# Optimization experiments

Hardware: AMD Instinct MI355X
Metric: run time of the kernel (lower is better)

The kernel has to match this reference:

```python
import jax, jax.numpy as jnp
import numpy as np
import math

WH, WW = 7, 7          # window size
N = WH * WW            # tokens per window = 49
H = 12                 # num heads
C = 384                # dim
D = C // H             # head dim = 32
NW = 64                # num windows (56x56 map, 7x7 windows)
B = 32                 # image batch
BW = B * NW            # windowed batch = 2048


def _cpb_constants():
    # log-spaced continuous relative coords table, flattened to [(2*WH-1)*(2*WW-1), 2]
    rh = np.arange(-(WH - 1), WH, dtype=np.float32)
    rw = np.arange(-(WW - 1), WW, dtype=np.float32)
    t = np.stack(np.meshgrid(rh, rw, indexing='ij'), axis=-1)  # [13,13,2]
    t[..., 0] /= (WH - 1)
    t[..., 1] /= (WW - 1)
    t *= 8.0
    t = np.sign(t) * np.log2(np.abs(t) + 1.0) / np.log2(8.0)
    # relative position index [N*N]
    ch, cw = np.meshgrid(np.arange(WH), np.arange(WW), indexing='ij')
    cf = np.stack([ch.ravel(), cw.ravel()])            # [2, N]
    rel = cf[:, :, None] - cf[:, None, :]              # [2, N, N]
    rel = rel.transpose(1, 2, 0).astype(np.int64)      # [N, N, 2]
    rel[..., 0] += WH - 1
    rel[..., 1] += WW - 1
    rel[..., 0] *= 2 * WW - 1
    rpi = rel.sum(-1).reshape(-1)                      # [N*N]
    return jnp.asarray(t.reshape(-1, 2)), jnp.asarray(rpi)

_COORDS_TABLE, _RPI = _cpb_constants()


def setup_inputs() -> dict:
    key = jax.random.key(0)
    ks = jax.random.split(key, 8)
    x = jax.random.normal(ks[0], (BW, N, C), dtype=jnp.float32)
    # shifted-window style 0/-100 mask
    mask = jnp.where(jax.random.uniform(ks[1], (NW, N, N)) < 0.1, -100.0, 0.0).astype(jnp.float32)
    qkv_w = jax.random.normal(ks[2], (3 * C, C), dtype=jnp.float32) * 0.02
    q_bias = jnp.zeros((C,), dtype=jnp.float32)
    v_bias = jnp.zeros((C,), dtype=jnp.float32)
    logit_scale = jnp.full((H, 1, 1), math.log(10.0), dtype=jnp.float32)
    cpb_w1 = jax.random.normal(ks[3], (512, 2), dtype=jnp.float32) * 0.02
    cpb_b1 = jnp.zeros((512,), dtype=jnp.float32)
    cpb_w2 = jax.random.normal(ks[4], (H, 512), dtype=jnp.float32) * 0.02
    proj_w = jax.random.normal(ks[5], (C, C), dtype=jnp.float32) * 0.02
    proj_b = jnp.zeros((C,), dtype=jnp.float32)
    return {"x": x, "mask": mask, "qkv_w": qkv_w, "q_bias": q_bias, "v_bias": v_bias,
            "logit_scale": logit_scale, "cpb_w1": cpb_w1, "cpb_b1": cpb_b1,
            "cpb_w2": cpb_w2, "proj_w": proj_w, "proj_b": proj_b}


def reference(x, mask, qkv_w, q_bias, v_bias, logit_scale, cpb_w1, cpb_b1, cpb_w2, proj_w, proj_b):
    B_, n, c = x.shape
    # qkv projection; k has no bias (registered zeros buffer)
    qkv_bias = jnp.concatenate([q_bias, jnp.zeros_like(q_bias), v_bias])
    qkv = x @ qkv_w.T + qkv_bias                              # [B_, N, 3C]
    qkv = qkv.reshape(B_, n, 3, H, D).transpose(2, 0, 3, 1, 4)  # [3, B_, H, N, D]
    q, k, v = qkv[0], qkv[1], qkv[2]
    # cosine attention
    qn = q / jnp.clip(jnp.linalg.norm(q, axis=-1, keepdims=True), 1e-12)
    kn = k / jnp.clip(jnp.linalg.norm(k, axis=-1, keepdims=True), 1e-12)
    attn = jnp.einsum('bhnd,bhmd->bhnm', qn, kn)              # [B_, H, N, N]
    scale = jnp.exp(jnp.minimum(logit_scale, math.log(1.0 / 0.01)))  # [H,1,1]
    attn = attn * scale
    # continuous position bias MLP + gather
    hid = jax.nn.relu(_COORDS_TABLE @ cpb_w1.T + cpb_b1)      # [169, 512]
    bias_tab = hid @ cpb_w2.T                                  # [169, H]
    rpb = bias_tab[_RPI].reshape(n, n, H).transpose(2, 0, 1)  # [H, N, N]
    rpb = 16.0 * jax.nn.sigmoid(rpb)
    attn = attn + rpb[None]
    # shifted-window mask add
    nW = mask.shape[0]
    attn = attn.reshape(B_ // nW, nW, H, n, n) + mask[None, :, None]
    attn = jax.nn.softmax(attn.reshape(B_, H, n, n), axis=-1)
    out = jnp.einsum('bhnm,bhmd->bnhd', attn, v).reshape(B_, n, c)
    return out @ proj_w.T + proj_b
```

## Files before the change

### kernel.cpp

```cpp
#include <hip/hip_runtime.h>
#include <hip/hip_bf16.h>
#include <math.h>

#define NTOK 49
#define NH 12
#define HD 32
#define CDIM 384
#define NWIN 64
#define BWIN 2048

typedef __bf16 bf16x8 __attribute__((ext_vector_type(8)));
typedef __bf16 bf16x4 __attribute__((ext_vector_type(4)));
typedef float f32x4 __attribute__((ext_vector_type(4)));

__device__ __forceinline__ void gload_lds16(const void* g, void* l) {
    __builtin_amdgcn_global_load_lds((const __attribute__((address_space(1))) void*)g,
                                     (__attribute__((address_space(3))) void*)l, 16, 0, 0);
}

__global__ void cvt_f32_bf16(const float* __restrict__ src, __bf16* __restrict__ dst, int n8) {
    int i = blockIdx.x * blockDim.x + threadIdx.x;
    if (i >= n8) return;
    f32x4 a = *(const f32x4*)(src + (size_t)i * 8);
    f32x4 b = *(const f32x4*)(src + (size_t)i * 8 + 4);
    bf16x8 o;
#pragma unroll
    for (int e = 0; e < 4; ++e) { o[e] = (__bf16)a[e]; o[e + 4] = (__bf16)b[e]; }
    *(bf16x8*)(dst + (size_t)i * 8) = o;
}

__global__ void cpb_mlp_kernel(const float* __restrict__ w1, const float* __restrict__ b1,
                               const float* __restrict__ w2, float* __restrict__ bias_tab) {
    int t = blockIdx.x * blockDim.x + threadIdx.x;
    if (t >= 169 * NH) return;
    int r = t / NH, h = t - (t / NH) * NH;
    int i = r / 13, j = r - (r / 13) * 13;
    float a0 = (float)(i - 6) * (8.0f / 6.0f);
    float a1 = (float)(j - 6) * (8.0f / 6.0f);
    float c0 = copysignf(log2f(fabsf(a0) + 1.0f) * (1.0f / 3.0f), a0);
    float c1 = copysignf(log2f(fabsf(a1) + 1.0f) * (1.0f / 3.0f), a1);
    float sum = 0.f;
    for (int k = 0; k < 512; ++k) {
        float hid = c0 * w1[2 * k] + c1 * w1[2 * k + 1] + b1[k];
        hid = fmaxf(hid, 0.f);
        sum += hid * w2[h * 512 + k];
    }
    bias_tab[r * NH + h] = sum;
}

__global__ void rpbT_kernel(const float* __restrict__ bias_tab, float* __restrict__ rpbT) {
    int idx = blockIdx.x * blockDim.x + threadIdx.x;
    if (idx >= NH * NTOK * NTOK) return;
    int h = idx / (NTOK * NTOK);
    int rem = idx - h * (NTOK * NTOK);
    int kj = rem / NTOK, qi = rem - (rem / NTOK) * NTOK;
    int chi = qi / 7, cwi = qi - chi * 7;
    int chj = kj / 7, cwj = kj - chj * 7;
    int rpi = (chi - chj + 6) * 13 + (cwi - cwj + 6);
    float x = bias_tab[rpi * NH + h];
    rpbT[idx] = 16.f / (1.f + __expf(-x));
}

__global__ void maskT_kernel(const float* __restrict__ mask, float* __restrict__ maskT) {
    int idx = blockIdx.x * blockDim.x + threadIdx.x;
    if (idx >= NWIN * NTOK * NTOK) return;
    int w = idx / (NTOK * NTOK);
    int rem = idx - w * (NTOK * NTOK);
    int kj = rem / NTOK, qi = rem - (rem / NTOK) * NTOK;
    maskT[idx] = mask[(w * NTOK + qi) * NTOK + kj];
}

template <int MODE, int NBY>
__global__ __launch_bounds__(256) void gemm4(
    const __bf16* __restrict__ A, const __bf16* __restrict__ Bw,
    const float* __restrict__ qbias, const float* __restrict__ vbias,
    __bf16* __restrict__ qkvout,
    float* __restrict__ fout, const float* __restrict__ fbias)
{
    __shared__ __bf16 As[3][128 * 32];
    __shared__ __bf16 Bs[3][128 * 32];
    const int tid = threadIdx.x;
    const int chunk = (784 * NBY) >> 3;
    const int wg = (blockIdx.x & 7) * chunk + (blockIdx.x >> 3);
    const int gx = wg / NBY, gy = wg - (wg / NBY) * NBY;
    const int lane = tid & 63;
    const int wid = tid >> 6;
    const int wr = (wid >> 1) * 64;
    const int wc = (wid & 1) * 64;
    const int fr = lane & 15;
    const int fq = lane >> 4;

    f32x4 acc[4][4];
#pragma unroll
    for (int m = 0; m < 4; ++m)
#pragma unroll
        for (int n = 0; n < 4; ++n)
            acc[m][n] = (f32x4){0.f, 0.f, 0.f, 0.f};

    const int srow0 = tid >> 2, scp0 = tid & 3;
    const int srow1 = (256 + tid) >> 2, scp1 = tid & 3;
    const size_t ar0 = (size_t)(gx * 128 + srow0) * CDIM + (scp0 ^ ((srow0 >> 1) & 3)) * 8;
    const size_t ar1 = (size_t)(gx * 128 + srow1) * CDIM + (scp1 ^ ((srow1 >> 1) & 3)) * 8;
    const size_t br0 = (size_t)(gy * 128 + srow0) * CDIM + (scp0 ^ ((srow0 >> 1) & 3)) * 8;
    const size_t br1 = (size_t)(gy * 128 + srow1) * CDIM + (scp1 ^ ((srow1 >> 1) & 3)) * 8;
    const int ls0 = tid * 16, ls1 = (256 + tid) * 16;

#define STAGE4(ti, buf) do {                                            \
        const int kk_ = (ti) * 32;                                      \
        gload_lds16(A + ar0 + kk_, (char*)&As[buf][0] + ls0);           \
        gload_lds16(A + ar1 + kk_, (char*)&As[buf][0] + ls1);           \
        gload_lds16(Bw + br0 + kk_, (char*)&Bs[buf][0] + ls0);          \
        gload_lds16(Bw + br1 + kk_, (char*)&Bs[buf][0] + ls1);          \
    } while (0)

    STAGE4(0, 0);
    STAGE4(1, 1);

#pragma unroll
    for (int t = 0; t < 12; ++t) {
        if (t < 11) asm volatile("s_waitcnt vmcnt(4)" ::: "memory");
        else        asm volatile("s_waitcnt vmcnt(0)" ::: "memory");
        __builtin_amdgcn_s_barrier();
        if (t + 2 < 12) STAGE4(t + 2, (t + 2) % 3);
        const int cur = t % 3;
        bf16x8 af[4], bfr[4];
#pragma unroll
        for (int m = 0; m < 4; ++m) {
            const int row = wr + m * 16 + fr;
            af[m] = *(const bf16x8*)&As[cur][row * 32 + (fq ^ ((row >> 1) & 3)) * 8];
        }
#pragma unroll
        for (int n = 0; n < 4; ++n) {
            const int row = wc + n * 16 + fr;
            bfr[n] = *(const bf16x8*)&Bs[cur][row * 32 + (fq ^ ((row >> 1) & 3)) * 8];
        }
#pragma unroll
        for (int m = 0; m < 4; ++m)
#pragma unroll
            for (int n = 0; n < 4; ++n)
                acc[m][n] = __builtin_amdgcn_mfma_f32_16x16x32_bf16(af[m], bfr[n], acc[m][n], 0, 0, 0);
    }
#undef STAGE4

    if (MODE == 0) {
        const int colbase = gy * 128;
        const int part = colbase / CDIM;
        const int pcolbase = colbase - part * CDIM;
        __bf16* dst = qkvout + (size_t)part * ((size_t)BWIN * NH * NTOK * HD);
#pragma unroll
        for (int m = 0; m < 4; ++m) {
#pragma unroll
            for (int r = 0; r < 4; ++r) {
                const int row = gx * 128 + wr + m * 16 + fq * 4 + r;
                const int b = row / NTOK;
                const int nn = row - b * NTOK;
#pragma unroll
                for (int n = 0; n < 4; ++n) {
                    const int pcol = pcolbase + wc + n * 16 + fr;
                    float val = acc[m][n][r];
                    if (part == 0) val += qbias[pcol];
                    if (part == 2) val += vbias[pcol];
                    const int h = pcol >> 5, d = pcol & 31;
                    dst[(((size_t)b * NH + h) * NTOK + nn) * HD + d] = (__bf16)val;
                }
            }
        }
    } else {
#pragma unroll
        for (int m = 0; m < 4; ++m) {
#pragma unroll
            for (int r = 0; r < 4; ++r) {
                const int row = gx * 128 + wr + m * 16 + fq * 4 + r;
                float* orow = fout + (size_t)row * CDIM + gy * 128 + wc;
#pragma unroll
                for (int n = 0; n < 4; ++n) {
                    const int col = gy * 128 + wc + n * 16 + fr;
                    orow[n * 16 + fr] = acc[m][n][r] + fbias[col];
                }
            }
        }
    }
}

#define WREG 15872
__global__ __launch_bounds__(256) void attn2(
    const __bf16* __restrict__ qb, const __bf16* __restrict__ kb,
    const __bf16* __restrict__ vb, const float* __restrict__ maskT,
    const float* __restrict__ rpbT, const float* __restrict__ lscale,
    __bf16* __restrict__ aout)
{
    __shared__ char smem[4 * WREG];
    const int tid = threadIdx.x;
    const int wid = tid >> 6, lane = tid & 63;
    const int bh = blockIdx.x * 4 + wid;
    const int b = bh / NH, h = bh - b * NH;
    const int w = b & (NWIN - 1);
    const int c = lane & 15, g = lane >> 4;

    char* base = smem + wid * WREG;
    __bf16* Kl = (__bf16*)base;
    __bf16* Ql = (__bf16*)(base + 5120);
    __bf16* Vl = (__bf16*)(base + 10240);
    float* invq = (float*)(base + 15360);
    float* invk = (float*)(base + 15616);
    __bf16* Pl = (__bf16*)base;

    const float sc = __expf(fminf(lscale[h], 4.6051702f));

    {
        const int row = lane;
        const size_t rb = (size_t)bh * (NTOK * HD) + (size_t)row * HD;
        bf16x8 z;
#pragma unroll
        for (int e = 0; e < 8; ++e) z[e] = (__bf16)0.f;
        {
            bf16x8 t[4];
            float ss = 0.f;
            if (row < NTOK) {
#pragma unroll
                for (int ch = 0; ch < 4; ++ch) {
                    t[ch] = *(const bf16x8*)(qb + rb + ch * 8);
#pragma unroll
                    for (int e = 0; e < 8; ++e) { float f = (float)t[ch][e]; ss += f * f; }
                }
            } else {
#pragma unroll
                for (int ch = 0; ch < 4; ++ch) t[ch] = z;
            }
#pragma unroll
            for (int ch = 0; ch < 4; ++ch) *(bf16x8*)&Ql[row * 40 + ch * 8] = t[ch];
            invq[row] = sc / fmaxf(sqrtf(ss), 1e-12f);
        }
        {
            bf16x8 t[4];
            float ss = 0.f;
            if (row < NTOK) {
#pragma unroll
                for (int ch = 0; ch < 4; ++ch) {
                    t[ch] = *(const bf16x8*)(kb + rb + ch * 8);
#pragma unroll
                    for (int e = 0; e < 8; ++e) { float f = (float)t[ch][e]; ss += f * f; }
                }
            } else {
#pragma unroll
                for (int ch = 0; ch < 4; ++ch) t[ch] = z;
            }
#pragma unroll
            for (int ch = 0; ch < 4; ++ch) *(bf16x8*)&Kl[row * 40 + ch * 8] = t[ch];
            invk[row] = 1.f / fmaxf(sqrtf(ss), 1e-12f);
        }
        {
            bf16x8 t[4];
            if (row < NTOK) {
#pragma unroll
                for (int ch = 0; ch < 4; ++ch) t[ch] = *(const bf16x8*)(vb + rb + ch * 8);
            } else {
#pragma unroll
                for (int ch = 0; ch < 4; ++ch) t[ch] = z;
            }
#pragma unroll
            for (int ch = 0; ch < 4; ++ch) *(bf16x8*)&Vl[row * 40 + ch * 8] = t[ch];
        }
    }

    bf16x8 kfr[4], qfr[4];
#pragma unroll
    for (int mt = 0; mt < 4; ++mt) kfr[mt] = *(const bf16x8*)&Kl[(mt * 16 + c) * 40 + g * 8];
#pragma unroll
    for (int nt = 0; nt < 4; ++nt) qfr[nt] = *(const bf16x8*)&Ql[(nt * 16 + c) * 40 + g * 8];
    f32x4 S[4][4];
#pragma unroll
    for (int mt = 0; mt < 4; ++mt)
#pragma unroll
        for (int nt = 0; nt < 4; ++nt) {
            S[mt][nt] = (f32x4){0.f, 0.f, 0.f, 0.f};
            S[mt][nt] = __builtin_amdgcn_mfma_f32_16x16x32_bf16(kfr[mt], qfr[nt], S[mt][nt], 0, 0, 0);
        }

    const float* rp = rpbT + h * (NTOK * NTOK);
    const float* mk = maskT + w * (NTOK * NTOK);
    float ivq[4];
#pragma unroll
    for (int nt = 0; nt < 4; ++nt) ivq[nt] = invq[nt * 16 + c];
#pragma unroll
    for (int mt = 0; mt < 4; ++mt) {
#pragma unroll
        for (int r = 0; r < 4; ++r) {
            const int k = mt * 16 + g * 4 + r;
            const float ivk = invk[k];
#pragma unroll
            for (int nt = 0; nt < 4; ++nt) {
                const int q = nt * 16 + c;
                float v = S[mt][nt][r] * ivk * ivq[nt];
                if (k < NTOK) {
                    if (q < NTOK) v += rp[k * NTOK + q] + mk[k * NTOK + q];
                } else {
                    v = -1e30f;
                }
                S[mt][nt][r] = v;
            }
        }
    }

    float rs[4];
#pragma unroll
    for (int nt = 0; nt < 4; ++nt) {
        float m = -1e30f;
#pragma unroll
        for (int mt = 0; mt < 4; ++mt)
#pragma unroll
            for (int r = 0; r < 4; ++r) m = fmaxf(m, S[mt][nt][r]);
        m = fmaxf(m, __shfl_xor(m, 16));
        m = fmaxf(m, __shfl_xor(m, 32));
        float s = 0.f;
#pragma unroll
        for (int mt = 0; mt < 4; ++mt)
#pragma unroll
            for (int r = 0; r < 4; ++r) {
                float e = __expf(S[mt][nt][r] - m);
                S[mt][nt][r] = e;
                s += e;
            }
        s += __shfl_xor(s, 16);
        s += __shfl_xor(s, 32);
        rs[nt] = 1.f / s;
    }

#pragma unroll
    for (int mt = 0; mt < 4; ++mt)
#pragma unroll
        for (int nt = 0; nt < 4; ++nt) {
            bf16x4 pk;
#pragma unroll
            for (int r = 0; r < 4; ++r) pk[r] = (__bf16)(S[mt][nt][r] * rs[nt]);
            *(bf16x4*)((char*)Pl + (nt * 16 + c) * 144 + (mt * 16 + g * 4) * 2) = pk;
        }

    bf16x8 vfr[2][2];
#pragma unroll
    for (int kt = 0; kt < 2; ++kt)
#pragma unroll
        for (int dt = 0; dt < 2; ++dt) {
            bf16x8 t;
#pragma unroll
            for (int e = 0; e < 8; ++e) t[e] = Vl[(kt * 32 + g * 8 + e) * 40 + dt * 16 + c];
            vfr[kt][dt] = t;
        }
    f32x4 O[4][2];
#pragma unroll
    for (int mt = 0; mt < 4; ++mt)
#pragma unroll
        for (int dt = 0; dt < 2; ++dt) O[mt][dt] = (f32x4){0.f, 0.f, 0.f, 0.f};
#pragma unroll
    for (int mt = 0; mt < 4; ++mt)
#pragma unroll
        for (int kt = 0; kt < 2; ++kt) {
            bf16x8 pfr = *(const bf16x8*)((char*)Pl + (mt * 16 + c) * 144 + kt * 64 + g * 16);
#pragma unroll
            for (int dt = 0; dt < 2; ++dt)
                O[mt][dt] = __builtin_amdgcn_mfma_f32_16x16x32_bf16(pfr, vfr[kt][dt], O[mt][dt], 0, 0, 0);
        }

#pragma unroll
    for (int mt = 0; mt < 4; ++mt)
#pragma unroll
        for (int r = 0; r < 4; ++r) {
            const int q = mt * 16 + g * 4 + r;
            if (q < NTOK) {
                const size_t off = ((size_t)b * NTOK + q) * CDIM + h * HD;
                aout[off + c] = (__bf16)O[mt][0][r];
                aout[off + 16 + c] = (__bf16)O[mt][1][r];
            }
        }
}

extern "C" void kernel_launch(void* const* d_in, const int* in_sizes, int n_in,
                              void* d_out, int out_size, void* d_ws, size_t ws_size,
                              hipStream_t stream) {
    const float* x      = (const float*)d_in[0];
    const float* mask   = (const float*)d_in[1];
    const float* qkv_w  = (const float*)d_in[2];
    const float* q_bias = (const float*)d_in[3];
    const float* v_bias = (const float*)d_in[4];
    const float* lscale = (const float*)d_in[5];
    const float* cpb_w1 = (const float*)d_in[6];
    const float* cpb_b1 = (const float*)d_in[7];
    const float* cpb_w2 = (const float*)d_in[8];
    const float* proj_w = (const float*)d_in[9];
    const float* proj_b = (const float*)d_in[10];
    float* out = (float*)d_out;

    const size_t QKVELEMS = (size_t)BWIN * NH * NTOK * HD;
    __bf16* qkvbuf  = (__bf16*)d_ws;
    __bf16* xbf     = qkvbuf + 3 * QKVELEMS;
    __bf16* aoutbuf = xbf;
    __bf16* qkv_wb  = xbf + QKVELEMS;
    __bf16* proj_wb = qkv_wb + 1152 * CDIM;
    float*  bias_tab = (float*)(proj_wb + CDIM * CDIM);
    float*  rpbT   = bias_tab + 169 * NH;
    float*  maskT  = rpbT + NH * NTOK * NTOK;

    hipLaunchKernelGGL(cvt_f32_bf16, dim3((int)((QKVELEMS / 8 + 255) / 256)), dim3(256), 0, stream,
                       x, xbf, (int)(QKVELEMS / 8));
    hipLaunchKernelGGL(cvt_f32_bf16, dim3((1152 * CDIM / 8 + 255) / 256), dim3(256), 0, stream,
                       qkv_w, qkv_wb, 1152 * CDIM / 8);
    hipLaunchKernelGGL(cvt_f32_bf16, dim3((CDIM * CDIM / 8 + 255) / 256), dim3(256), 0, stream,
                       proj_w, proj_wb, CDIM * CDIM / 8);
    hipLaunchKernelGGL(cpb_mlp_kernel, dim3(8), dim3(256), 0, stream,
                       cpb_w1, cpb_b1, cpb_w2, bias_tab);
    hipLaunchKernelGGL(rpbT_kernel, dim3((NH * NTOK * NTOK + 255) / 256), dim3(256), 0, stream,
                       bias_tab, rpbT);
    hipLaunchKernelGGL(maskT_kernel, dim3((NWIN * NTOK * NTOK + 255) / 256), dim3(256), 0, stream,
                       mask, maskT);
    hipLaunchKernelGGL((gemm4<0, 9>), dim3(784 * 9), dim3(256), 0, stream,
                       xbf, qkv_wb, q_bias, v_bias, qkvbuf, (float*)nullptr,
                       (const float*)nullptr);
    hipLaunchKernelGGL(attn2, dim3(BWIN * NH / 4), dim3(256), 0, stream,
                       qkvbuf, qkvbuf + QKVELEMS, qkvbuf + 2 * QKVELEMS, maskT, rpbT, lscale,
                       aoutbuf);
    hipLaunchKernelGGL((gemm4<1, 3>), dim3(784 * 3), dim3(256), 0, stream,
                       aoutbuf, proj_wb, (const float*)nullptr, (const float*)nullptr,
                       (__bf16*)nullptr, out, proj_b);
}
```

Before: 462.4 us.

## Fuse fp32-to-bf16 conversion of x into QKV GEMM A-tile loading

```diff
diff --git a/kernel.cpp b/kernel.cpp
--- a/kernel.cpp
+++ b/kernel.cpp
@@ -70,19 +70,17 @@
     maskT[idx] = mask[(w * NTOK + qi) * NTOK + kj];
 }
 
-template <int MODE, int NBY>
-__global__ __launch_bounds__(256) void gemm4(
-    const __bf16* __restrict__ A, const __bf16* __restrict__ Bw,
+__global__ __launch_bounds__(256) void gemm_qkv(
+    const float* __restrict__ X, const __bf16* __restrict__ Bw,
     const float* __restrict__ qbias, const float* __restrict__ vbias,
-    __bf16* __restrict__ qkvout,
-    float* __restrict__ fout, const float* __restrict__ fbias)
+    __bf16* __restrict__ qkvout)
 {
     __shared__ __bf16 As[3][128 * 32];
     __shared__ __bf16 Bs[3][128 * 32];
     const int tid = threadIdx.x;
-    const int chunk = (784 * NBY) >> 3;
+    const int chunk = (784 * 9) >> 3;
     const int wg = (blockIdx.x & 7) * chunk + (blockIdx.x >> 3);
-    const int gx = wg / NBY, gy = wg - (wg / NBY) * NBY;
+    const int gx = wg / 9, gy = wg - (wg / 9) * 9;
     const int lane = tid & 63;
     const int wid = tid >> 6;
     const int wr = (wid >> 1) * 64;
@@ -97,31 +95,159 @@
         for (int n = 0; n < 4; ++n)
             acc[m][n] = (f32x4){0.f, 0.f, 0.f, 0.f};
 
+    const int arow = tid >> 1, ahalf = tid & 1;
+    const float* aptr = X + (size_t)(gx * 128 + arow) * CDIM + ahalf * 16;
+    const int aswz = (arow >> 1) & 3;
+    const int ap0 = (ahalf * 2) ^ aswz;
+    const int ap1 = (ahalf * 2 + 1) ^ aswz;
+
     const int srow0 = tid >> 2, scp0 = tid & 3;
-    const int srow1 = (256 + tid) >> 2, scp1 = tid & 3;
+    const int srow1 = (256 + tid) >> 2;
+    const size_t br0 = (size_t)(gy * 128 + srow0) * CDIM + (scp0 ^ ((srow0 >> 1) & 3)) * 8;
+    const size_t br1 = (size_t)(gy * 128 + srow1) * CDIM + (scp0 ^ ((srow1 >> 1) & 3)) * 8;
+    const int ls0 = tid * 16, ls1 = (256 + tid) * 16;
+
+    f32x4 av0, av1, av2, av3;
+#define ALOAD(ti) do {                                \
+        av0 = *(const f32x4*)(aptr + (ti) * 32);      \
+        av1 = *(const f32x4*)(aptr + (ti) * 32 + 4);  \
+        av2 = *(const f32x4*)(aptr + (ti) * 32 + 8);  \
+        av3 = *(const f32x4*)(aptr + (ti) * 32 + 12); \
+    } while (0)
+#define AWRITE(buf) do {                                                 \
+        bf16x8 c0, c1;                                                   \
+        for (int e = 0; e < 4; ++e) {                                    \
+            c0[e] = (__bf16)av0[e]; c0[e + 4] = (__bf16)av1[e];          \
+            c1[e] = (__bf16)av2[e]; c1[e + 4] = (__bf16)av3[e];          \
+        }                                                                \
+        *(bf16x8*)&As[buf][arow * 32 + ap0 * 8] = c0;                    \
+        *(bf16x8*)&As[buf][arow * 32 + ap1 * 8] = c1;                    \
+    } while (0)
+#define BSTAGE(ti, buf) do {                                             \
+        const int kk_ = (ti) * 32;                                       \
+        gload_lds16(Bw + br0 + kk_, (char*)&Bs[buf][0] + ls0);           \
+        gload_lds16(Bw + br1 + kk_, (char*)&Bs[buf][0] + ls1);           \
+    } while (0)
+
+    ALOAD(0);
+    BSTAGE(0, 0);
+    {
+        f32x4 t0 = av0, t1 = av1, t2 = av2, t3 = av3;
+        ALOAD(1);
+        BSTAGE(1, 1);
+        f32x4 s0 = av0, s1 = av1, s2 = av2, s3 = av3;
+        av0 = t0; av1 = t1; av2 = t2; av3 = t3;
+        asm volatile("s_waitcnt vmcnt(8)" ::: "memory");
+        AWRITE(0);
+        av0 = s0; av1 = s1; av2 = s2; av3 = s3;
+    }
+
+#pragma unroll
+    for (int t = 0; t < 12; ++t) {
+        if (t < 11) asm volatile("s_waitcnt vmcnt(2)" ::: "memory");
+        else        asm volatile("s_waitcnt vmcnt(0)" ::: "memory");
+        asm volatile("s_waitcnt lgkmcnt(0)" ::: "memory");
+        __builtin_amdgcn_s_barrier();
+        if (t + 1 < 12) AWRITE((t + 1) % 3);
+        if (t + 2 < 12) {
+            ALOAD(t + 2);
+            BSTAGE(t + 2, (t + 2) % 3);
+        }
+        const int cur = t % 3;
+        bf16x8 af[4], bfr[4];
+#pragma unroll
+        for (int m = 0; m < 4; ++m) {
+            const int row = wr + m * 16 + fr;
+            af[m] = *(const bf16x8*)&As[cur][row * 32 + (fq ^ ((row >> 1) & 3)) * 8];
+        }
+#pragma unroll
+        for (int n = 0; n < 4; ++n) {
+            const int row = wc + n * 16 + fr;
+            bfr[n] = *(const bf16x8*)&Bs[cur][row * 32 + (fq ^ ((row >> 1) & 3)) * 8];
+        }
+#pragma unroll
+        for (int m = 0; m < 4; ++m)
+#pragma unroll
+            for (int n = 0; n < 4; ++n)
+                acc[m][n] = __builtin_amdgcn_mfma_f32_16x16x32_bf16(af[m], bfr[n], acc[m][n], 0, 0, 0);
+    }
+#undef ALOAD
+#undef AWRITE
+#undef BSTAGE
+
+    const int colbase = gy * 128;
+    const int part = colbase / CDIM;
+    const int pcolbase = colbase - part * CDIM;
+    __bf16* dst = qkvout + (size_t)part * ((size_t)BWIN * NH * NTOK * HD);
+#pragma unroll
+    for (int m = 0; m < 4; ++m) {
+#pragma unroll
+        for (int r = 0; r < 4; ++r) {
+            const int row = gx * 128 + wr + m * 16 + fq * 4 + r;
+            const int b = row / NTOK;
+            const int nn = row - b * NTOK;
+#pragma unroll
+            for (int n = 0; n < 4; ++n) {
+                const int pcol = pcolbase + wc + n * 16 + fr;
+                float val = acc[m][n][r];
+                if (part == 0) val += qbias[pcol];
+                if (part == 2) val += vbias[pcol];
+                const int h = pcol >> 5, d = pcol & 31;
+                dst[(((size_t)b * NH + h) * NTOK + nn) * HD + d] = (__bf16)val;
+            }
+        }
+    }
+}
+
+__global__ __launch_bounds__(256) void gemm_proj(
+    const __bf16* __restrict__ A, const __bf16* __restrict__ Bw,
+    float* __restrict__ fout, const float* __restrict__ fbias)
+{
+    __shared__ __bf16 As[3][128 * 32];
+    __shared__ __bf16 Bs[3][128 * 32];
+    const int tid = threadIdx.x;
+    const int chunk = (784 * 3) >> 3;
+    const int wg = (blockIdx.x & 7) * chunk + (blockIdx.x >> 3);
+    const int gx = wg / 3, gy = wg - (wg / 3) * 3;
+    const int lane = tid & 63;
+    const int wid = tid >> 6;
+    const int wr = (wid >> 1) * 64;
+    const int wc = (wid & 1) * 64;
+    const int fr = lane & 15;
+    const int fq = lane >> 4;
+
+    f32x4 acc[4][4];
+#pragma unroll
+    for (int m = 0; m < 4; ++m)
+#pragma unroll
+        for (int n = 0; n < 4; ++n)
+            acc[m][n] = (f32x4){0.f, 0.f, 0.f, 0.f};
+
+    const int srow0 = tid >> 2, scp0 = tid & 3;
+    const int srow1 = (256 + tid) >> 2;
     const size_t ar0 = (size_t)(gx * 128 + srow0) * CDIM + (scp0 ^ ((srow0 >> 1) & 3)) * 8;
-    const size_t ar1 = (size_t)(gx * 128 + srow1) * CDIM + (scp1 ^ ((srow1 >> 1) & 3)) * 8;
+    const size_t ar1 = (size_t)(gx * 128 + srow1) * CDIM + (scp0 ^ ((srow1 >> 1) & 3)) * 8;
     const size_t br0 = (size_t)(gy * 128 + srow0) * CDIM + (scp0 ^ ((srow0 >> 1) & 3)) * 8;
-    const size_t br1 = (size_t)(gy * 128 + srow1) * CDIM + (scp1 ^ ((srow1 >> 1) & 3)) * 8;
+    const size_t br1 = (size_t)(gy * 128 + srow1) * CDIM + (scp0 ^ ((srow1 >> 1) & 3)) * 8;
     const int ls0 = tid * 16, ls1 = (256 + tid) * 16;
 
-#define STAGE4(ti, buf) do {                                            \
-        const int kk_ = (ti) * 32;                                      \
-        gload_lds16(A + ar0 + kk_, (char*)&As[buf][0] + ls0);           \
-        gload_lds16(A + ar1 + kk_, (char*)&As[buf][0] + ls1);           \
-        gload_lds16(Bw + br0 + kk_, (char*)&Bs[buf][0] + ls0);          \
-        gload_lds16(Bw + br1 + kk_, (char*)&Bs[buf][0] + ls1);          \
+#define STAGE(ti, buf) do {                                              \
+        const int kk_ = (ti) * 32;                                       \
+        gload_lds16(A + ar0 + kk_, (char*)&As[buf][0] + ls0);            \
+        gload_lds16(A + ar1 + kk_, (char*)&As[buf][0] + ls1);            \
+        gload_lds16(Bw + br0 + kk_, (char*)&Bs[buf][0] + ls0);           \
+        gload_lds16(Bw + br1 + kk_, (char*)&Bs[buf][0] + ls1);           \
     } while (0)
 
-    STAGE4(0, 0);
-    STAGE4(1, 1);
+    STAGE(0, 0);
+    STAGE(1, 1);
 
 #pragma unroll
     for (int t = 0; t < 12; ++t) {
         if (t < 11) asm volatile("s_waitcnt vmcnt(4)" ::: "memory");
         else        asm volatile("s_waitcnt vmcnt(0)" ::: "memory");
         __builtin_amdgcn_s_barrier();
-        if (t + 2 < 12) STAGE4(t + 2, (t + 2) % 3);
+        if (t + 2 < 12) STAGE(t + 2, (t + 2) % 3);
         const int cur = t % 3;
         bf16x8 af[4], bfr[4];
 #pragma unroll
@@ -140,43 +266,18 @@
             for (int n = 0; n < 4; ++n)
                 acc[m][n] = __builtin_amdgcn_mfma_f32_16x16x32_bf16(af[m], bfr[n], acc[m][n], 0, 0, 0);
     }
-#undef STAGE4
-
-    if (MODE == 0) {
-        const int colbase = gy * 128;
-        const int part = colbase / CDIM;
-        const int pcolbase = colbase - part * CDIM;
-        __bf16* dst = qkvout + (size_t)part * ((size_t)BWIN * NH * NTOK * HD);
-#pragma unroll
-        for (int m = 0; m < 4; ++m) {
-#pragma unroll
-            for (int r = 0; r < 4; ++r) {
-                const int row = gx * 128 + wr + m * 16 + fq * 4 + r;
-                const int b = row / NTOK;
-                const int nn = row - b * NTOK;
-#pragma unroll
-                for (int n = 0; n < 4; ++n) {
-                    const int pcol = pcolbase + wc + n * 16 + fr;
-                    float val = acc[m][n][r];
-                    if (part == 0) val += qbias[pcol];
-                    if (part == 2) val += vbias[pcol];
-                    const int h = pcol >> 5, d = pcol & 31;
-                    dst[(((size_t)b * NH + h) * NTOK + nn) * HD + d] = (__bf16)val;
-                }
-            }
-        }
-    } else {
-#pragma unroll
-        for (int m = 0; m < 4; ++m) {
-#pragma unroll
-            for (int r = 0; r < 4; ++r) {
-                const int row = gx * 128 + wr + m * 16 + fq * 4 + r;
-                float* orow = fout + (size_t)row * CDIM + gy * 128 + wc;
-#pragma unroll
-                for (int n = 0; n < 4; ++n) {
-                    const int col = gy * 128 + wc + n * 16 + fr;
-                    orow[n * 16 + fr] = acc[m][n][r] + fbias[col];
-                }
+#undef STAGE
+
+#pragma unroll
+    for (int m = 0; m < 4; ++m) {
+#pragma unroll
+        for (int r = 0; r < 4; ++r) {
+            const int row = gx * 128 + wr + m * 16 + fq * 4 + r;
+            float* orow = fout + (size_t)row * CDIM + gy * 128 + wc;
+#pragma unroll
+            for (int n = 0; n < 4; ++n) {
+                const int col = gy * 128 + wc + n * 16 + fr;
+                orow[n * 16 + fr] = acc[m][n][r] + fbias[col];
             }
         }
     }
@@ -203,7 +304,7 @@
     __bf16* Vl = (__bf16*)(base + 10240);
     float* invq = (float*)(base + 15360);
     float* invk = (float*)(base + 15616);
-    __bf16* Pl = (__bf16*)base;
+    char* Pl = base;
 
     const float sc = __expf(fminf(lscale[h], 4.6051702f));
 
@@ -333,7 +434,7 @@
             bf16x4 pk;
 #pragma unroll
             for (int r = 0; r < 4; ++r) pk[r] = (__bf16)(S[mt][nt][r] * rs[nt]);
-            *(bf16x4*)((char*)Pl + (nt * 16 + c) * 144 + (mt * 16 + g * 4) * 2) = pk;
+            *(bf16x4*)(Pl + (nt * 16 + c) * 144 + (mt * 16 + g * 4) * 2) = pk;
         }
 
     bf16x8 vfr[2][2];
@@ -355,7 +456,7 @@
     for (int mt = 0; mt < 4; ++mt)
 #pragma unroll
         for (int kt = 0; kt < 2; ++kt) {
-            bf16x8 pfr = *(const bf16x8*)((char*)Pl + (mt * 16 + c) * 144 + kt * 64 + g * 16);
+            bf16x8 pfr = *(const bf16x8*)(Pl + (mt * 16 + c) * 144 + kt * 64 + g * 16);
 #pragma unroll
             for (int dt = 0; dt < 2; ++dt)
                 O[mt][dt] = __builtin_amdgcn_mfma_f32_16x16x32_bf16(pfr, vfr[kt][dt], O[mt][dt], 0, 0, 0);
@@ -392,16 +493,13 @@
 
     const size_t QKVELEMS = (size_t)BWIN * NH * NTOK * HD;
     __bf16* qkvbuf  = (__bf16*)d_ws;
-    __bf16* xbf     = qkvbuf + 3 * QKVELEMS;
-    __bf16* aoutbuf = xbf;
-    __bf16* qkv_wb  = xbf + QKVELEMS;
+    __bf16* aoutbuf = qkvbuf + 3 * QKVELEMS;
+    __bf16* qkv_wb  = aoutbuf + QKVELEMS;
     __bf16* proj_wb = qkv_wb + 1152 * CDIM;
     float*  bias_tab = (float*)(proj_wb + CDIM * CDIM);
     float*  rpbT   = bias_tab + 169 * NH;
     float*  maskT  = rpbT + NH * NTOK * NTOK;
 
-    hipLaunchKernelGGL(cvt_f32_bf16, dim3((int)((QKVELEMS / 8 + 255) / 256)), dim3(256), 0, stream,
-                       x, xbf, (int)(QKVELEMS / 8));
     hipLaunchKernelGGL(cvt_f32_bf16, dim3((1152 * CDIM / 8 + 255) / 256), dim3(256), 0, stream,
                        qkv_w, qkv_wb, 1152 * CDIM / 8);
     hipLaunchKernelGGL(cvt_f32_bf16, dim3((CDIM * CDIM / 8 + 255) / 256), dim3(256), 0, stream,
@@ -412,13 +510,11 @@
                        bias_tab, rpbT);
     hipLaunchKernelGGL(maskT_kernel, dim3((NWIN * NTOK * NTOK + 255) / 256), dim3(256), 0, stream,
                        mask, maskT);
-    hipLaunchKernelGGL((gemm4<0, 9>), dim3(784 * 9), dim3(256), 0, stream,
-                       xbf, qkv_wb, q_bias, v_bias, qkvbuf, (float*)nullptr,
-                       (const float*)nullptr);
+    hipLaunchKernelGGL(gemm_qkv, dim3(784 * 9), dim3(256), 0, stream,
+                       x, qkv_wb, q_bias, v_bias, qkvbuf);
     hipLaunchKernelGGL(attn2, dim3(BWIN * NH / 4), dim3(256), 0, stream,
                        qkvbuf, qkvbuf + QKVELEMS, qkvbuf + 2 * QKVELEMS, maskT, rpbT, lscale,
                        aoutbuf);
-    hipLaunchKernelGGL((gemm4<1, 3>), dim3(784 * 3), dim3(256), 0, stream,
-                       aoutbuf, proj_wb, (const float*)nullptr, (const float*)nullptr,
-                       (__bf16*)nullptr, out, proj_b);
-}
+    hipLaunchKernelGGL(gemm_proj, dim3(784 * 3), dim3(256), 0, stream,
+                       aoutbuf, proj_wb, out, proj_b);
+}
```

Result: slower. 526.5 us (+13.9%).
